# Kernel tuning notes

Hardware: AMD Instinct MI355X
Metric: run time of the kernel (lower is better)

The kernel has to match this reference:

```python
import jax, jax.numpy as jnp
import numpy as np

NUM_HEADS = 4
GROUPS = 8
EPS = 1e-5


def setup_inputs() -> dict:
    key = jax.random.key(0)
    ks = jax.random.split(key, 8)
    B, C, H, W = 8, 512, 64, 64
    L, E = 77, 768
    std = 0.02
    return {
        "x": jax.random.normal(ks[0], (B, C, H, W), jnp.float32),
        "text_emb": jax.random.normal(ks[1], (B, L, E), jnp.float32),
        "attention_mask": jax.random.randint(ks[2], (B, L), 0, 2, jnp.int32),
        "Wq_w": jax.random.normal(ks[3], (C, C), jnp.float32) * std,
        "Wq_b": jnp.zeros((C,), jnp.float32),
        "Wk_w": jax.random.normal(ks[4], (C, E), jnp.float32) * std,
        "Wk_b": jnp.zeros((C,), jnp.float32),
        "Wv_w": jax.random.normal(ks[5], (C, E), jnp.float32) * std,
        "Wv_b": jnp.zeros((C,), jnp.float32),
        "gn_scale": jnp.ones((C,), jnp.float32),
        "gn_bias": jnp.zeros((C,), jnp.float32),
    }


def reference(x, text_emb, attention_mask, Wq_w, Wq_b, Wk_w, Wk_b, Wv_w, Wv_b, gn_scale, gn_bias):
    B, C, H, W = x.shape
    dh = C // NUM_HEADS
    scale = dh ** -0.5

    # [B, HW, C] queries from image features
    x_flat = x.reshape(B, C, H * W).transpose(0, 2, 1)
    Q = x_flat @ Wq_w.T + Wq_b                 # [B, S, C]
    K = text_emb @ Wk_w.T + Wk_b               # [B, L, C]
    V = text_emb @ Wv_w.T + Wv_b               # [B, L, C]

    def split_heads(t):
        Bt, T, _ = t.shape
        return t.reshape(Bt, T, NUM_HEADS, dh).transpose(0, 2, 1, 3)  # [B, h, T, dh]

    Qh, Kh, Vh = split_heads(Q), split_heads(K), split_heads(V)

    scores = jnp.einsum("bhqd,bhkd->bhqk", Qh, Kh) * scale  # [B, h, S, L]
    mask = (attention_mask == 0)[:, None, None, :]
    scores = jnp.where(mask, -jnp.inf, scores)
    probs = jax.nn.softmax(scores, axis=-1)
    # dropout layers are identity in eval mode
    attn = jnp.einsum("bhqk,bhkd->bhqd", probs, Vh)          # [B, h, S, dh]

    out = attn.transpose(0, 2, 1, 3).reshape(B, H * W, C)    # [B, S, C]
    out = out.transpose(0, 2, 1).reshape(B, C, H, W)

    # GroupNorm(8 groups, affine) over (C/G, H, W) per group
    g = out.reshape(B, GROUPS, -1)
    mean = g.mean(axis=-1, keepdims=True)
    var = g.var(axis=-1, keepdims=True)
    g = (g - mean) * jax.lax.rsqrt(var + EPS)
    out = g.reshape(B, C, H, W) * gn_scale[None, :, None, None] + gn_bias[None, :, None, None]
    return out
```

## Files before the change

kernel.cpp:

```cpp
#include <hip/hip_runtime.h>
#include <hip/hip_bf16.h>
#include <cstdint>


typedef __attribute__((ext_vector_type(8))) short short8;
typedef __attribute__((ext_vector_type(4))) short short4v;
typedef __attribute__((ext_vector_type(4))) float f32x4;

#define DEV __device__ __forceinline__

DEV float bf2f(unsigned short u){ union{uint32_t i; float f;} x; x.i = ((uint32_t)u) << 16; return x.f; }
DEV unsigned short f2bf(float f){ __hip_bfloat16 h = __float2bfloat16(f); return *reinterpret_cast<unsigned short*>(&h); }
DEV short8 ld8(const unsigned short* p){ return *reinterpret_cast<const short8*>(p); }
DEV f32x4 ldf4(const float* p){ return *reinterpret_cast<const f32x4*>(p); }

#if defined(__has_builtin)
#if __has_builtin(__builtin_amdgcn_global_load_lds)
#define HAVE_ASYNC_LDS 1
#endif
#endif

__global__ __launch_bounds__(256) void k_fat(const float* __restrict__ x,
                                             unsigned short* __restrict__ xT,
                                             const float* __restrict__ text,
                                             const float* __restrict__ Wk,
                                             const float* __restrict__ Wkb,
                                             const float* __restrict__ Wv,
                                             const float* __restrict__ Wvb,
                                             unsigned short* __restrict__ wsK,
                                             unsigned short* __restrict__ wsVt,
                                             const float* __restrict__ Wq,
                                             unsigned short* __restrict__ wsWqT,
                                             int b0, int s_base, int slen, int SB){
  __shared__ unsigned short U[10368];
  const int tid = threadIdx.x;
  const int bx = blockIdx.x, by = blockIdx.y, bz = blockIdx.z;
  const int bg = b0 + bz;

  if (bx < 64){
    if (bx * 64 >= slen) return;
    unsigned short* t = U;
    const int s0 = s_base + bx * 64, c0 = by * 64;
    #pragma unroll
    for (int it = 0; it < 2; ++it){
      int slot = tid + it * 256;
      int r = slot >> 3, sg = slot & 7;
      int sw = sg ^ (r >> 3);
      const float* src = &x[((size_t)(bg * 512 + c0 + r)) * 4096 + s0 + sg * 8];
      f32x4 a = ldf4(src), b = ldf4(src + 4);
      short8 v;
      #pragma unroll
      for (int j = 0; j < 4; ++j){ v[j] = (short)f2bf(a[j]); v[j + 4] = (short)f2bf(b[j]); }
      *reinterpret_cast<short8*>(&t[r * 72 + sw * 8]) = v;
    }
    __syncthreads();
    #pragma unroll
    for (int it = 0; it < 2; ++it){
      int slot = tid + it * 256;
      int j = slot >> 3, i8 = slot & 7;
      short8 v;
      #pragma unroll
      for (int q = 0; q < 8; ++q){
        int c = i8 * 8 + q;
        int sw = (j >> 3) ^ i8;
        v[q] = (short)t[c * 72 + sw * 8 + (j & 7)];
      }
      *reinterpret_cast<short8*>(&xT[((size_t)(bz * slen) + bx * 64 + j) * 512 + c0 + i8 * 8]) = v;
    }
  } else if (bx < 66){
    unsigned short* At = U;
    unsigned short* Bt = U + 5760;
    const int wave = tid >> 6, lane = tid & 63;
    const int m16 = lane & 15, quad = lane >> 4;
    const int uc = (bx - 64) * 8 + by;
    const int u0 = uc * 64;
    const bool isK = (u0 < 512);
    const float* W  = isK ? Wk  : Wv;
    const float* Wb = isK ? Wkb : Wvb;
    const int c0 = u0 & 511;
    const int c  = c0 + wave * 16 + m16;
    f32x4 acc[5];
    #pragma unroll
    for (int mt = 0; mt < 5; ++mt) acc[mt] = (f32x4){0.f, 0.f, 0.f, 0.f};
    for (int kc = 0; kc < 12; ++kc){
      const int e0 = kc * 64;
      #pragma unroll
      for (int it = 0; it < 9; ++it){
        int slot = tid + it * 256;
        if (slot < 1280){
          int row = slot >> 4, e4 = (slot & 15) * 4;
          f32x4 v = (row < 77) ? ldf4(&text[((size_t)(bg * 77 + row)) * 768 + e0 + e4])
                               : (f32x4){0.f, 0.f, 0.f, 0.f};
          short4v o;
          #pragma unroll
          for (int j = 0; j < 4; ++j) o[j] = (short)f2bf(v[j]);
          *reinterpret_cast<short4v*>(&At[row * 72 + e4]) = o;
        } else {
          int bs = slot - 1280;
          int row = bs >> 4, e4 = (bs & 15) * 4;
          f32x4 v = ldf4(&W[((size_t)(c0 + row)) * 768 + e0 + e4]);
          short4v o;
          #pragma unroll
          for (int j = 0; j < 4; ++j) o[j] = (short)f2bf(v[j]);
          *reinterpret_cast<short4v*>(&Bt[row * 72 + e4]) = o;
        }
      }
      __syncthreads();
      #pragma unroll
      for (int kk = 0; kk < 64; kk += 32){
        short8 bf_ = *reinterpret_cast<const short8*>(&Bt[(wave * 16 + m16) * 72 + kk + quad * 8]);
        #pragma unroll
        for (int mt = 0; mt < 5; ++mt){
          short8 af_ = *reinterpret_cast<const short8*>(&At[(mt * 16 + m16) * 72 + kk + quad * 8]);
          acc[mt] = __builtin_amdgcn_mfma_f32_16x16x32_bf16(af_, bf_, acc[mt], 0, 0, 0);
        }
      }
      __syncthreads();
    }
    const float bias = Wb[c];
    if (isK){
      #pragma unroll
      for (int mt = 0; mt < 5; ++mt)
        #pragma unroll
        for (int r = 0; r < 4; ++r){
          int l = mt * 16 + quad * 4 + r;
          if (l < 77) wsK[((size_t)(bz * 77 + l)) * 512 + c] = f2bf(acc[mt][r] + bias);
        }
    } else {
      unsigned short* vr = &wsVt[((size_t)(bz * 512 + c)) * 96];
      #pragma unroll
      for (int mt = 0; mt < 5; ++mt){
        short4v pk;
        #pragma unroll
        for (int r = 0; r < 4; ++r) pk[r] = (short)f2bf(acc[mt][r] + bias);
        *reinterpret_cast<short4v*>(&vr[mt * 16 + quad * 4]) = pk;
      }
      short4v z = {};
      *reinterpret_cast<short4v*>(&vr[80 + quad * 4]) = z;
    }
  } else {
    unsigned short* t = U;
    const int nb = 8 * SB;
    const int p  = by + bz * 8;
    for (int tile = p; tile < 64; tile += nb){
      const int ti = tile >> 3, tj = tile & 7;
      #pragma unroll
      for (int it = 0; it < 2; ++it){
        int slot = tid + it * 256;
        int r = slot >> 3, sg = slot & 7;
        int sw = sg ^ (r >> 3);
        const float* src = &Wq[((size_t)(tj * 64 + r)) * 512 + ti * 64 + sg * 8];
        f32x4 a = ldf4(src), b2 = ldf4(src + 4);
        short8 v;
        #pragma unroll
        for (int j = 0; j < 4; ++j){ v[j] = (short)f2bf(a[j]); v[j + 4] = (short)f2bf(b2[j]); }
        *reinterpret_cast<short8*>(&t[r * 72 + sw * 8]) = v;
      }
      __syncthreads();
      #pragma unroll
      for (int it = 0; it < 2; ++it){
        int slot = tid + it * 256;
        int j = slot >> 3, i8 = slot & 7;
        short8 v;
        #pragma unroll
        for (int q = 0; q < 8; ++q){
          int dd = i8 * 8 + q;
          int sw = (j >> 3) ^ i8;
          v[q] = (short)t[dd * 72 + sw * 8 + (j & 7)];
        }
        *reinterpret_cast<short8*>(&wsWqT[((size_t)(ti * 64 + j)) * 512 + tj * 64 + i8 * 8]) = v;
      }
      __syncthreads();
    }
  }
}

__global__ __launch_bounds__(256) void k1b(const unsigned short* __restrict__ wsWqT,
                                           const unsigned short* __restrict__ wsK,
                                           const float* __restrict__ Wqb,
                                           unsigned short* __restrict__ wsKWq,
                                           float* __restrict__ kbias){
  const int tid = threadIdx.x;
  const int wave = tid >> 6, lane = tid & 63;
  const int m16 = lane & 15, quad = lane >> 4;
  const int cq = blockIdx.x, h = blockIdx.y, bz = blockIdx.z;
  const int cbase = cq * 128 + wave * 32;

  f32x4 acc[2][5];
  #pragma unroll
  for (int mt = 0; mt < 2; ++mt)
    #pragma unroll
    for (int nt = 0; nt < 5; ++nt) acc[mt][nt] = (f32x4){0.f, 0.f, 0.f, 0.f};

  #pragma unroll
  for (int ks = 0; ks < 4; ++ks){
    short8 aw[2];
    #pragma unroll
    for (int mt = 0; mt < 2; ++mt)
      aw[mt] = ld8(&wsWqT[(size_t)(cbase + mt * 16 + m16) * 512 + h * 128 + ks * 32 + quad * 8]);
    #pragma unroll
    for (int nt = 0; nt < 5; ++nt){
      int l = nt * 16 + m16;
      short8 bk = {};
      if (l < 77) bk = ld8(&wsK[((size_t)(bz * 77 + l)) * 512 + h * 128 + ks * 32 + quad * 8]);
      #pragma unroll
      for (int mt = 0; mt < 2; ++mt)
        acc[mt][nt] = __builtin_amdgcn_mfma_f32_16x16x32_bf16(aw[mt], bk, acc[mt][nt], 0, 0, 0);
    }
  }
  #pragma unroll
  for (int mt = 0; mt < 2; ++mt)
    #pragma unroll
    for (int nt = 0; nt < 5; ++nt){
      int l = nt * 16 + m16;
      short4v pk;
      #pragma unroll
      for (int r = 0; r < 4; ++r) pk[r] = (short)f2bf(acc[mt][nt][r]);
      *reinterpret_cast<short4v*>(&wsKWq[((size_t)((bz * 4 + h) * 80 + l)) * 512 + cbase + mt * 16 + quad * 4]) = pk;
    }
  if (cq == 0 && tid < 80){
    int l = tid;
    float kb = 0.f;
    if (l < 77){
      #pragma unroll
      for (int d = 0; d < 128; d += 8){
        short8 kv = ld8(&wsK[((size_t)(bz * 77 + l)) * 512 + h * 128 + d]);
        f32x4 wa = ldf4(&Wqb[h * 128 + d]);
        f32x4 wb = ldf4(&Wqb[h * 128 + d + 4]);
        #pragma unroll
        for (int j = 0; j < 4; ++j){
          kb += bf2f((unsigned short)kv[j]) * wa[j];
          kb += bf2f((unsigned short)kv[j + 4]) * wb[j];
        }
      }
    }
    kbias[(bz * 4 + h) * 80 + l] = kb;
  }
}

__global__ __launch_bounds__(256, 4) void k2_attn(const unsigned short* __restrict__ xT,
                                                  const unsigned short* __restrict__ wsKWq,
                                                  const unsigned short* __restrict__ wsVt,
                                                  const int* __restrict__ amask,
                                                  const float* __restrict__ kbias,
                                                  float* __restrict__ out,
                                                  float* __restrict__ gnacc,
                                                  int b0, int s_base, int slen){
  __shared__ unsigned short arena[13312];
  __shared__ float maskf[96];
  unsigned short* Pt = arena;

  const int tid = threadIdx.x;
  const int wave = tid >> 6, lane = tid & 63;
  const int m16 = lane & 15, quad = lane >> 4;
  const int bz = blockIdx.x, h = blockIdx.y, st = blockIdx.z;
  const int bg = b0 + bz;
  const int s_glob = s_base + st * 128;
  const int R0 = (wave >> 1) * 64, C0 = (wave & 1) * 64;
  const int sw0 = wave * 32;
  const float scale = 0.08838834764831845f;

  if (tid < 96){
    int l = tid;
    float mbv = -30000.f;
    if (l < 77 && amask[bg * 77 + l] != 0) mbv = kbias[(bz * 4 + h) * 80 + l] * scale;
    maskf[l] = mbv;
  }

  const unsigned short* Abase = wsKWq + (size_t)((bz * 4 + h) * 80) * 512;
  const unsigned short* Bbase = xT + ((size_t)bz * slen + st * 128 + sw0) * 512;

  f32x4 acc2[5][2];
  #pragma unroll
  for (int mt = 0; mt < 5; ++mt){ acc2[mt][0] = (f32x4){0.f,0.f,0.f,0.f}; acc2[mt][1] = (f32x4){0.f,0.f,0.f,0.f}; }

  auto stageA = [&](int kc, int buf){
    const int sbase = buf * 5120;
    #pragma unroll
    for (int it = 0; it < 3; ++it){
      const int ubase = it * 256 + wave * 64;
      if (ubase < 640){
        const int u = ubase + lane;
        int l = u >> 3, pos = (u & 7) ^ (l & 7);
        const unsigned short* src = Abase + (size_t)l * 512 + kc * 64 + pos * 8;
#ifdef HAVE_ASYNC_LDS
        __builtin_amdgcn_global_load_lds((const __attribute__((address_space(1))) void*)src,
                                         (__attribute__((address_space(3))) void*)&arena[sbase + ubase * 8],
                                         16, 0, 0);
#else
        *reinterpret_cast<short8*>(&arena[sbase + u * 8]) = ld8(src);
#endif
      }
    }
  };

  short8 Breg[2][4];
  auto loadB = [&](int kc, int buf){
    #pragma unroll
    for (int nt = 0; nt < 2; ++nt)
      #pragma unroll
      for (int kk = 0; kk < 2; ++kk)
        Breg[buf][nt * 2 + kk] = ld8(&Bbase[(size_t)(nt * 16 + m16) * 512 + kc * 64 + kk * 32 + quad * 8]);
  };

  auto compute = [&](int buf){
    const int ab = buf * 5120;
    #pragma unroll
    for (int kk = 0; kk < 2; ++kk){
      short8 af[5];
      #pragma unroll
      for (int mt = 0; mt < 5; ++mt){
        int l = mt * 16 + m16;
        int p = (kk * 4 + quad) ^ (l & 7);
        af[mt] = *reinterpret_cast<const short8*>(&arena[ab + l * 64 + p * 8]);
      }
      #pragma unroll
      for (int mt = 0; mt < 5; ++mt)
        #pragma unroll
        for (int nt = 0; nt < 2; ++nt)
          acc2[mt][nt] = __builtin_amdgcn_mfma_f32_16x16x32_bf16(af[mt], Breg[buf][nt * 2 + kk], acc2[mt][nt], 0, 0, 0);
    }
  };

  stageA(0, 0);
  loadB(0, 0);
  __syncthreads();
  #pragma unroll
  for (int kc = 0; kc < 8; ++kc){
    if (kc < 7){ stageA(kc + 1, (kc + 1) & 1); loadB(kc + 1, (kc + 1) & 1); }
    compute(kc & 1);
    __syncthreads();
  }

  const unsigned short* Vb = wsVt + (size_t)(bz * 512 + h * 128) * 96;
  short8 av0[4];
  #pragma unroll
  for (int mt = 0; mt < 4; ++mt)
    av0[mt] = ld8(&Vb[(size_t)(R0 + mt * 16 + m16) * 96 + quad * 8]);

  {
    float mb[5][4];
    #pragma unroll
    for (int mt = 0; mt < 5; ++mt)
      #pragma unroll
      for (int r = 0; r < 4; ++r) mb[mt][r] = maskf[mt * 16 + quad * 4 + r];
    #pragma unroll
    for (int nt = 0; nt < 2; ++nt){
      float sv[5][4]; float mx = -3e38f;
      #pragma unroll
      for (int mt = 0; mt < 5; ++mt)
        #pragma unroll
        for (int r = 0; r < 4; ++r){
          float v = acc2[mt][nt][r] * scale + mb[mt][r];
          sv[mt][r] = v; mx = fmaxf(mx, v);
        }
      mx = fmaxf(mx, __shfl_xor(mx, 16)); mx = fmaxf(mx, __shfl_xor(mx, 32));
      float sum = 0.f;
      #pragma unroll
      for (int mt = 0; mt < 5; ++mt)
        #pragma unroll
        for (int r = 0; r < 4; ++r){ float e = __expf(sv[mt][r] - mx); sv[mt][r] = e; sum += e; }
      sum += __shfl_xor(sum, 16); sum += __shfl_xor(sum, 32);
      float inv = 1.0f / sum;
      int sl = sw0 + nt * 16 + m16;
      #pragma unroll
      for (int mt = 0; mt < 5; ++mt){
        short4v pk;
        #pragma unroll
        for (int r = 0; r < 4; ++r) pk[r] = (short)f2bf(sv[mt][r] * inv);
        *reinterpret_cast<short4v*>(&Pt[sl * 104 + mt * 16 + quad * 4]) = pk;
      }
      short4v z = {};
      *reinterpret_cast<short4v*>(&Pt[sl * 104 + 80 + quad * 4]) = z;
    }
  }
  __syncthreads();

  f32x4 acc3[4][4];
  #pragma unroll
  for (int mt = 0; mt < 4; ++mt)
    #pragma unroll
    for (int nt = 0; nt < 4; ++nt) acc3[mt][nt] = (f32x4){0.f, 0.f, 0.f, 0.f};
  #pragma unroll
  for (int ks = 0; ks < 3; ++ks){
    short8 av[4], bp[4];
    #pragma unroll
    for (int mt = 0; mt < 4; ++mt)
      av[mt] = (ks == 0) ? av0[mt]
                         : ld8(&Vb[(size_t)(R0 + mt * 16 + m16) * 96 + ks * 32 + quad * 8]);
    #pragma unroll
    for (int nt = 0; nt < 4; ++nt)
      bp[nt] = *reinterpret_cast<const short8*>(&Pt[(C0 + nt * 16 + m16) * 104 + ks * 32 + quad * 8]);
    #pragma unroll
    for (int mt = 0; mt < 4; ++mt)
      #pragma unroll
      for (int nt = 0; nt < 4; ++nt)
        acc3[mt][nt] = __builtin_amdgcn_mfma_f32_16x16x32_bf16(av[mt], bp[nt], acc3[mt][nt], 0, 0, 0);
  }
  float sum = 0.f, ssq = 0.f;
  #pragma unroll
  for (int mt = 0; mt < 4; ++mt)
    #pragma unroll
    for (int nt = 0; nt < 4; ++nt){
      int sidx = s_glob + C0 + nt * 16 + m16;
      #pragma unroll
      for (int r = 0; r < 4; ++r){
        float v = acc3[mt][nt][r];
        sum += v; ssq += v * v;
        int d = h * 128 + R0 + mt * 16 + quad * 4 + r;
        out[(size_t)(bg * 512 + d) * 4096 + sidx] = v;
      }
    }
  #pragma unroll
  for (int off = 1; off < 64; off <<= 1){ sum += __shfl_xor(sum, off); ssq += __shfl_xor(ssq, off); }
  if (lane == 0){
    int g = h * 2 + (R0 >> 6);
    atomicAdd(&gnacc[(bg * 8 + g) * 2],     sum);
    atomicAdd(&gnacc[(bg * 8 + g) * 2 + 1], ssq);
  }
}

__global__ __launch_bounds__(256) void k3_gn(float* __restrict__ out,
                                             const float* __restrict__ gnacc,
                                             const float* __restrict__ gns,
                                             const float* __restrict__ gnb){
  const int bx = blockIdx.x;
  const int b = bx >> 9, c = bx & 511;
  const int g = c >> 6;
  const float s  = gnacc[(b * 8 + g) * 2];
  const float ss = gnacc[(b * 8 + g) * 2 + 1];
  const float invN = 1.f / 262144.f;
  const float mean = s * invN;
  const float var  = ss * invN - mean * mean;
  const float rstd = rsqrtf(fmaxf(var, 0.f) + 1e-5f);
  const float a  = rstd * gns[c];
  const float bb = gnb[c] - mean * a;
  const size_t base = (size_t)bx * 4096;
  #pragma unroll
  for (int p = 0; p < 4; ++p){
    size_t off = base + p * 1024 + threadIdx.x * 4;
    f32x4 v = ldf4(&out[off]);
    f32x4 o;
    #pragma unroll
    for (int j = 0; j < 4; ++j) o[j] = v[j] * a + bb;
    *reinterpret_cast<f32x4*>(&out[off]) = o;
  }
}

extern "C" void kernel_launch(void* const* d_in, const int* in_sizes, int n_in,
                              void* d_out, int out_size, void* d_ws, size_t ws_size,
                              hipStream_t stream){
  (void)in_sizes; (void)n_in; (void)out_size;
  const float* x    = (const float*)d_in[0];
  const float* text = (const float*)d_in[1];
  const int*   am   = (const int*)d_in[2];
  const float* Wq   = (const float*)d_in[3];
  const float* Wqb  = (const float*)d_in[4];
  const float* Wk   = (const float*)d_in[5];
  const float* Wkb  = (const float*)d_in[6];
  const float* Wv   = (const float*)d_in[7];
  const float* Wvb  = (const float*)d_in[8];
  const float* gns  = (const float*)d_in[9];
  const float* gnb  = (const float*)d_in[10];
  float* out = (float*)d_out;

  auto need = [](int SB, int SLEN) -> size_t {
    return 512ull + 524288ull + (size_t)SB * 506112ull + (size_t)SB * SLEN * 1024ull;
  };
  int SB = 8, SLEN = 4096;
  if      (ws_size >= need(8, 4096)) { SB = 8; SLEN = 4096; }
  else if (ws_size >= need(4, 4096)) { SB = 4; SLEN = 4096; }
  else if (ws_size >= need(2, 4096)) { SB = 2; SLEN = 4096; }
  else if (ws_size >= need(1, 4096)) { SB = 1; SLEN = 4096; }
  else if (ws_size >= need(1, 1024)) { SB = 1; SLEN = 1024; }
  else                               { SB = 1; SLEN = 256;  }

  uint8_t* ws = (uint8_t*)d_ws;
  float*          gnacc = (float*)ws;
  unsigned short* wsWqT = (unsigned short*)(ws + 512);
  unsigned short* wsK   = wsWqT + 512 * 512;
  unsigned short* wsVt  = wsK  + (size_t)SB * 77 * 512;
  unsigned short* wsKWq = wsVt + (size_t)SB * 512 * 96;
  float*          kbias = (float*)(wsKWq + (size_t)SB * 4 * 80 * 512);
  unsigned short* xT    = (unsigned short*)(kbias + (size_t)SB * 4 * 80);

  hipMemsetAsync(gnacc, 0, 128 * sizeof(float), stream);
  for (int b0 = 0; b0 < 8; b0 += SB){
    for (int s_base = 0; s_base < 4096; s_base += SLEN){
      k_fat<<<dim3(67, 8, SB), 256, 0, stream>>>(x, xT, text, Wk, Wkb, Wv, Wvb,
                                                 wsK, wsVt, Wq, wsWqT, b0, s_base, SLEN, SB);
      if (s_base == 0)
        k1b<<<dim3(4, 4, SB), 256, 0, stream>>>(wsWqT, wsK, Wqb, wsKWq, kbias);
      k2_attn<<<dim3(SB, 4, SLEN / 128), 256, 0, stream>>>(xT, wsKWq, wsVt, am, kbias,
                                                           out, gnacc, b0, s_base, SLEN);
    }
  }
  k3_gn<<<4096, 256, 0, stream>>>(out, gnacc, gns, gnb);
}
```

Measured before the change: 131.0 us.

## Store transposed bf16 x in channel-chunked layout and widen transpose tiles

The transpose stage in k_fat now writes the bf16 copy of x as [batch][channel-chunk of 64][s][64] rather than [s][512]. Each block now covers 256 spatial positions instead of 64, so the grid shrinks to SLEN/256+3 columns. The attention kernel's B-operand loads are re-indexed to this layout, giving each k-chunk a contiguous region for better locality and coalescing. The trade-offs are a larger LDS tile that lowers occupancy, 64-element per-thread register arrays, and LDS reads with a row stride of 264 that may cause bank conflicts.

```diff
diff --git a/kernel.cpp b/kernel.cpp
--- a/kernel.cpp
+++ b/kernel.cpp
@@ -21,7 +21,7 @@
 #endif
 
 __global__ __launch_bounds__(256) void k_fat(const float* __restrict__ x,
-                                             unsigned short* __restrict__ xT,
+                                             unsigned short* __restrict__ xTt,
                                              const float* __restrict__ text,
                                              const float* __restrict__ Wk,
                                              const float* __restrict__ Wkb,
@@ -32,47 +32,46 @@
                                              const float* __restrict__ Wq,
                                              unsigned short* __restrict__ wsWqT,
                                              int b0, int s_base, int slen, int SB){
-  __shared__ unsigned short U[10368];
+  __shared__ unsigned short U[16896];
   const int tid = threadIdx.x;
   const int bx = blockIdx.x, by = blockIdx.y, bz = blockIdx.z;
   const int bg = b0 + bz;
-
-  if (bx < 64){
-    if (bx * 64 >= slen) return;
-    unsigned short* t = U;
-    const int s0 = s_base + bx * 64, c0 = by * 64;
-    #pragma unroll
-    for (int it = 0; it < 2; ++it){
-      int slot = tid + it * 256;
-      int r = slot >> 3, sg = slot & 7;
-      int sw = sg ^ (r >> 3);
-      const float* src = &x[((size_t)(bg * 512 + c0 + r)) * 4096 + s0 + sg * 8];
-      f32x4 a = ldf4(src), b = ldf4(src + 4);
-      short8 v;
-      #pragma unroll
-      for (int j = 0; j < 4; ++j){ v[j] = (short)f2bf(a[j]); v[j + 4] = (short)f2bf(b[j]); }
-      *reinterpret_cast<short8*>(&t[r * 72 + sw * 8]) = v;
+  const int NT = slen >> 8;
+
+  if (bx < NT){
+    const int cc = by, c0 = cc * 64;
+    const int s0 = s_base + bx * 256;
+    {
+      const int r = tid >> 2, sub = tid & 3;
+      const float* src = &x[((size_t)(bg * 512 + c0 + r)) * 4096 + s0 + sub * 64];
+      unsigned short* drow = &U[r * 264 + sub * 64];
+      #pragma unroll
+      for (int i = 0; i < 8; ++i){
+        f32x4 a = ldf4(src + i * 8), b = ldf4(src + i * 8 + 4);
+        short8 v;
+        #pragma unroll
+        for (int j = 0; j < 4; ++j){ v[j] = (short)f2bf(a[j]); v[j + 4] = (short)f2bf(b[j]); }
+        *reinterpret_cast<short8*>(drow + i * 8) = v;
+      }
     }
     __syncthreads();
-    #pragma unroll
-    for (int it = 0; it < 2; ++it){
-      int slot = tid + it * 256;
-      int j = slot >> 3, i8 = slot & 7;
-      short8 v;
-      #pragma unroll
-      for (int q = 0; q < 8; ++q){
-        int c = i8 * 8 + q;
-        int sw = (j >> 3) ^ i8;
-        v[q] = (short)t[c * 72 + sw * 8 + (j & 7)];
-      }
-      *reinterpret_cast<short8*>(&xT[((size_t)(bz * slen) + bx * 64 + j) * 512 + c0 + i8 * 8]) = v;
-    }
-  } else if (bx < 66){
+    {
+      const int j = tid;
+      unsigned short v[64];
+      #pragma unroll
+      for (int r = 0; r < 64; ++r) v[r] = U[r * 264 + j];
+      const int sloc = bx * 256 + j;
+      unsigned short* dst = &xTt[(((size_t)bz * 8 + cc) * slen + sloc) * 64];
+      #pragma unroll
+      for (int g = 0; g < 8; ++g)
+        *reinterpret_cast<short8*>(dst + g * 8) = *reinterpret_cast<short8*>(&v[g * 8]);
+    }
+  } else if (bx < NT + 2){
     unsigned short* At = U;
     unsigned short* Bt = U + 5760;
     const int wave = tid >> 6, lane = tid & 63;
     const int m16 = lane & 15, quad = lane >> 4;
-    const int uc = (bx - 64) * 8 + by;
+    const int uc = (bx - NT) * 8 + by;
     const int u0 = uc * 64;
     const bool isK = (u0 < 512);
     const float* W  = isK ? Wk  : Wv;
@@ -238,7 +237,7 @@
   }
 }
 
-__global__ __launch_bounds__(256, 4) void k2_attn(const unsigned short* __restrict__ xT,
+__global__ __launch_bounds__(256, 4) void k2_attn(const unsigned short* __restrict__ xTt,
                                                   const unsigned short* __restrict__ wsKWq,
                                                   const unsigned short* __restrict__ wsVt,
                                                   const int* __restrict__ amask,
@@ -268,7 +267,8 @@
   }
 
   const unsigned short* Abase = wsKWq + (size_t)((bz * 4 + h) * 80) * 512;
-  const unsigned short* Bbase = xT + ((size_t)bz * slen + st * 128 + sw0) * 512;
+  const unsigned short* Bb    = xTt + (size_t)(bz * 8) * slen * 64;
+  const int srow0 = st * 128 + sw0;
 
   f32x4 acc2[5][2];
   #pragma unroll
@@ -296,11 +296,12 @@
 
   short8 Breg[2][4];
   auto loadB = [&](int kc, int buf){
+    const unsigned short* Bc = Bb + ((size_t)kc * slen + srow0) * 64;
     #pragma unroll
     for (int nt = 0; nt < 2; ++nt)
       #pragma unroll
       for (int kk = 0; kk < 2; ++kk)
-        Breg[buf][nt * 2 + kk] = ld8(&Bbase[(size_t)(nt * 16 + m16) * 512 + kc * 64 + kk * 32 + quad * 8]);
+        Breg[buf][nt * 2 + kk] = ld8(&Bc[(size_t)(nt * 16 + m16) * 64 + kk * 32 + quad * 8]);
   };
 
   auto compute = [&](int buf){
@@ -482,16 +483,17 @@
   unsigned short* wsVt  = wsK  + (size_t)SB * 77 * 512;
   unsigned short* wsKWq = wsVt + (size_t)SB * 512 * 96;
   float*          kbias = (float*)(wsKWq + (size_t)SB * 4 * 80 * 512);
-  unsigned short* xT    = (unsigned short*)(kbias + (size_t)SB * 4 * 80);
+  unsigned short* xTt   = (unsigned short*)(kbias + (size_t)SB * 4 * 80);
 
   hipMemsetAsync(gnacc, 0, 128 * sizeof(float), stream);
   for (int b0 = 0; b0 < 8; b0 += SB){
     for (int s_base = 0; s_base < 4096; s_base += SLEN){
-      k_fat<<<dim3(67, 8, SB), 256, 0, stream>>>(x, xT, text, Wk, Wkb, Wv, Wvb,
-                                                 wsK, wsVt, Wq, wsWqT, b0, s_base, SLEN, SB);
+      const int NT = SLEN >> 8;
+      k_fat<<<dim3(NT + 3, 8, SB), 256, 0, stream>>>(x, xTt, text, Wk, Wkb, Wv, Wvb,
+                                                     wsK, wsVt, Wq, wsWqT, b0, s_base, SLEN, SB);
       if (s_base == 0)
         k1b<<<dim3(4, 4, SB), 256, 0, stream>>>(wsWqT, wsK, Wqb, wsKWq, kbias);
-      k2_attn<<<dim3(SB, 4, SLEN / 128), 256, 0, stream>>>(xT, wsKWq, wsVt, am, kbias,
+      k2_attn<<<dim3(SB, 4, SLEN / 128), 256, 0, stream>>>(xTt, wsKWq, wsVt, am, kbias,
                                                            out, gnacc, b0, s_base, SLEN);
     }
   }
```

Measured after the change: 132.2 us. About the same (+0.9%).
